# Optimization experiments

Hardware: AMD Instinct MI355X
Metric: run time of the kernel (lower is better)

Reference implementation:

```python
import jax, jax.numpy as jnp
import numpy as np

K = 8  # in-edges per non-source node (forward direction)

def _mp_forward(y, src_local, pre_w, pre_b, upd_w, upd_b):
    # y: [L, P, D] node features by topological level; src_local: [L-1, P*K]
    L, P, D = y.shape
    # level 0 has no in-edges: builtin mean gives z = 0 -> y += relu(update(0)) = relu(b)
    y0 = jax.nn.relu(upd_b) + y[0]
    def step(y_prev, inp):
        src, y_init = inp
        msg = jax.nn.relu(y_prev[src] @ pre_w + pre_b)      # [P*K, D] gather + msg FNN
        z = msg.reshape(P, K, D).mean(axis=1)               # fn.mean reduce
        y_new = jax.nn.relu(z @ upd_w + upd_b) + y_init     # update + residual
        return y_new, y_new
    _, ys = jax.lax.scan(step, y0, (src_local, y[1:]))
    return jnp.concatenate([y0[None], ys], axis=0)

def _mp_reverse(y, src_local, pre_w, pre_b, upd_w, upd_b):
    # propagate along reversed edges, reverse topological order
    L, P, D = y.shape
    dst_local = jnp.repeat(jnp.arange(P), K)                # local dst of each fwd edge
    y_last = jax.nn.relu(upd_b) + y[-1]                     # sinks: z = 0
    def step(y_next, inp):
        src, y_init = inp
        msg = jax.nn.relu(y_next[dst_local] @ pre_w + pre_b)            # [P*K, D]
        z_sum = jax.ops.segment_sum(msg, src, num_segments=P)
        deg = jax.ops.segment_sum(jnp.ones((P * K,), msg.dtype), src, num_segments=P)
        z = z_sum / jnp.maximum(deg, 1.0)[:, None]          # mean; zero-deg -> 0
        y_new = jax.nn.relu(z @ upd_w + upd_b) + y_init
        return y_new, y_new
    _, ys = jax.lax.scan(step, y_last, (src_local, y[:-1]), reverse=True)
    return jnp.concatenate([ys, y_last[None]], axis=0)

def setup_inputs() -> dict:
    key = jax.random.key(0)
    ks = jax.random.split(key, 16)
    N, node_dim, D = 131072, 128, 128   # D = out_dim // 2
    L, P = 16, 8192
    s = 0.06
    return {
        "x": jax.random.normal(ks[0], (N, node_dim), jnp.float32),
        "src_local": jax.random.randint(ks[1], (L - 1, P * K), 0, P).astype(jnp.int32),
        "nt_w1": jax.random.normal(ks[2], (node_dim, node_dim), jnp.float32) * s,
        "nt_b1": jax.random.normal(ks[3], (node_dim,), jnp.float32) * s,
        "nt_w2": jax.random.normal(ks[4], (node_dim, D), jnp.float32) * s,
        "nt_b2": jax.random.normal(ks[5], (D,), jnp.float32) * s,
        "f_pre_w": jax.random.normal(ks[6], (D, D), jnp.float32) * s,
        "f_pre_b": jax.random.normal(ks[7], (D,), jnp.float32) * s,
        "f_upd_w": jax.random.normal(ks[8], (D, D), jnp.float32) * s,
        "f_upd_b": jax.random.normal(ks[9], (D,), jnp.float32) * s,
        "b_pre_w": jax.random.normal(ks[10], (D, D), jnp.float32) * s,
        "b_pre_b": jax.random.normal(ks[11], (D,), jnp.float32) * s,
        "b_upd_w": jax.random.normal(ks[12], (D, D), jnp.float32) * s,
        "b_upd_b": jax.random.normal(ks[13], (D,), jnp.float32) * s,
    }

def reference(x, src_local, nt_w1, nt_b1, nt_w2, nt_b2,
              f_pre_w, f_pre_b, f_upd_w, f_upd_b,
              b_pre_w, b_pre_b, b_upd_w, b_upd_b):
    Lm1, PK = src_local.shape
    P, L = PK // K, Lm1 + 1
    N = x.shape[0]
    # node_transform: FNN(node_dim, [node_dim], out_dim//2)
    h = jax.nn.relu(x @ nt_w1 + nt_b1) @ nt_w2 + nt_b2      # [N, D]
    y = h.reshape(L, P, -1)
    hf = _mp_forward(y, src_local, f_pre_w, f_pre_b, f_upd_w, f_upd_b).reshape(N, -1)
    hb = _mp_reverse(y, src_local, b_pre_w, b_pre_b, b_upd_w, b_upd_b).reshape(N, -1)
    return jnp.concatenate([hf, hb], axis=1)
```

## Files before the change

### kernel.cpp

```cpp
#include <hip/hip_runtime.h>
#include <cstddef>
#include <cstdint>

#define DD   128
#define PP   8192
#define KK   8
#define LLV  16
#define NN   131072
#define NE   65536
#define NLVL 15

typedef _Float16 h8 __attribute__((ext_vector_type(8)));
typedef _Float16 h4 __attribute__((ext_vector_type(4)));
typedef float f4v __attribute__((ext_vector_type(4)));

__device__ __forceinline__ float4 ld4(const float* p) { return *(const float4*)p; }
__device__ __forceinline__ void st4(float* p, float4 v) { *(float4*)p = v; }

__device__ __forceinline__ int swz(int row, int k) { return row * 128 + (k ^ ((row & 7) << 3)); }

__device__ __forceinline__ void hstore4(_Float16* ah, int row, int k0, float4 v) {
  int o = swz(row, k0);
  h4 hi;
  hi[0] = (_Float16)v.x; hi[1] = (_Float16)v.y;
  hi[2] = (_Float16)v.z; hi[3] = (_Float16)v.w;
  *(h4*)(ah + o) = hi;
}

__device__ __forceinline__ void load_bfrags1(const _Float16* __restrict__ img, int t16, int lane,
                                             h8 Bh[4], h8 Bl[4]) {
#pragma unroll
  for (int ks = 0; ks < 4; ks++) {
    int o = ((t16 * 4 + ks) * 64 + lane) * 8;
    Bh[ks] = *(const h8*)(img + o);
    Bl[ks] = *(const h8*)(img + 16384 + o);
  }
}

__device__ __forceinline__ f4v gemm_rt(const _Float16* __restrict__ ah,
                                       const h8 Bh[4], const h8 Bl[4], int rbase, int lane) {
  int r16 = lane & 15, kb = lane >> 4;
  int arow = rbase + r16;
  h8 Ah[4];
#pragma unroll
  for (int ks = 0; ks < 4; ks++) Ah[ks] = *(const h8*)(ah + swz(arow, ks * 32 + kb * 8));
  f4v a = {0.f, 0.f, 0.f, 0.f};
#pragma unroll
  for (int ks = 0; ks < 4; ks++) a = __builtin_amdgcn_mfma_f32_16x16x32_f16(Ah[ks], Bh[ks], a, 0, 0, 0);
#pragma unroll
  for (int ks = 0; ks < 4; ks++) a = __builtin_amdgcn_mfma_f32_16x16x32_f16(Ah[ks], Bl[ks], a, 0, 0, 0);
  return a;
}

__global__ __launch_bounds__(1024) void setup_kernel(
    const float* __restrict__ w0, const float* __restrict__ w1,
    const float* __restrict__ w2, const float* __restrict__ w3,
    const float* __restrict__ w4, const float* __restrict__ w5,
    _Float16* __restrict__ img_base,
    const int* __restrict__ src_all,
    int* __restrict__ offs, int* __restrict__ edges) {
  int t = threadIdx.x;
  if (blockIdx.x < 12) {
    int mat = blockIdx.x >> 1;
    int g = (blockIdx.x & 1) * 1024 + t;
    const float* w;
    switch (mat) {
      case 0: w = w0; break;
      case 1: w = w1; break;
      case 2: w = w2; break;
      case 3: w = w3; break;
      case 4: w = w4; break;
      default: w = w5; break;
    }
    _Float16* img = img_base + (size_t)mat * 32768;
    int t16 = g >> 8, ks = (g >> 6) & 3, lane = g & 63;
    int n = t16 * 16 + (lane & 15);
    int kb = ks * 32 + (lane >> 4) * 8;
    h8 hi, lo;
#pragma unroll
    for (int j = 0; j < 8; j++) {
      float v = w[(kb + j) * 128 + n];
      _Float16 h = (_Float16)v;
      hi[j] = h;
      lo[j] = (_Float16)(v - (float)h);
    }
    int o = ((t16 * 4 + ks) * 64 + lane) * 8;
    *(h8*)(img + o) = hi;
    *(h8*)(img + 16384 + o) = lo;
  } else {
    int l = blockIdx.x - 12;
    const int* src = src_all + (size_t)l * NE;
    __shared__ int cnt[PP];
    __shared__ int bsum[1024];
#pragma unroll
    for (int j = 0; j < 8; j++) cnt[t + j * 1024] = 0;
    __syncthreads();
#pragma unroll 4
    for (int j = 0; j < 64; j++) {
      int q = src[j * 1024 + t];
      atomicAdd(&cnt[q], 1);
    }
    __syncthreads();
    int loc[8];
    int s = 0;
#pragma unroll
    for (int j = 0; j < 8; j++) { loc[j] = cnt[t * 8 + j]; s += loc[j]; }
    bsum[t] = s;
    __syncthreads();
    for (int off = 1; off < 1024; off <<= 1) {
      int v = (t >= off) ? bsum[t - off] : 0;
      __syncthreads();
      bsum[t] += v;
      __syncthreads();
    }
    int run = (t == 0) ? 0 : bsum[t - 1];
#pragma unroll
    for (int j = 0; j < 8; j++) {
      offs[l * (PP + 1) + t * 8 + j] = run;
      cnt[t * 8 + j] = run;
      run += loc[j];
    }
    if (t == 1023) offs[l * (PP + 1) + PP] = run;
    __syncthreads();
#pragma unroll 4
    for (int j = 0; j < 64; j++) {
      int e = j * 1024 + t;
      int q = src[e];
      int pos = atomicAdd(&cnt[q], 1);
      edges[(size_t)l * NE + pos] = e >> 3;
    }
  }
}

__global__ __launch_bounds__(512, 4) void nt_kernel(
    const float* __restrict__ x,
    const _Float16* __restrict__ w1img, const float* __restrict__ b1,
    const _Float16* __restrict__ w2img, const float* __restrict__ b2,
    float* __restrict__ hout,
    const float* __restrict__ f_upd_b, const _Float16* __restrict__ f_pre_img,
    const float* __restrict__ f_pre_b,
    const float* __restrict__ b_upd_b, const _Float16* __restrict__ b_pre_img,
    const float* __restrict__ b_pre_b,
    _Float16* __restrict__ mf0, _Float16* __restrict__ mb0,
    float* __restrict__ out) {
  __shared__ __align__(16) _Float16 abuf0[8192];
  __shared__ __align__(16) _Float16 abuf1[8192];
  int tid = threadIdx.x;
  int lane = tid & 63, wv = tid >> 6;
  int r16 = lane & 15, kb = lane >> 4;
  int colg = wv * 16 + r16;
  size_t base = (size_t)blockIdx.x * 64;

  h8 Bh[4], Bl[4];
  load_bfrags1(w1img, wv, lane, Bh, Bl);

#pragma unroll
  for (int j = 0; j < 4; j++) {
    int s = tid + j * 512;
    float4 v = ((const float4*)(x + base * 128))[s];
    hstore4(abuf0, s >> 5, (s & 31) * 4, v);
  }
  __syncthreads();

  f4v acc[4];
#pragma unroll
  for (int rt = 0; rt < 4; rt++) acc[rt] = gemm_rt(abuf0, Bh, Bl, rt * 16, lane);
  load_bfrags1(w2img, wv, lane, Bh, Bl);
  {
    float b = b1[colg];
#pragma unroll
    for (int rt = 0; rt < 4; rt++)
#pragma unroll
      for (int r = 0; r < 4; r++)
        abuf1[swz(rt * 16 + kb * 4 + r, colg)] = (_Float16)fmaxf(acc[rt][r] + b, 0.f);
  }
  __syncthreads();

#pragma unroll
  for (int rt = 0; rt < 4; rt++) acc[rt] = gemm_rt(abuf1, Bh, Bl, rt * 16, lane);
  float b2s = b2[colg];
#pragma unroll
  for (int rt = 0; rt < 4; rt++)
#pragma unroll
    for (int r = 0; r < 4; r++) {
      int row = rt * 16 + kb * 4 + r;
      hout[(base + row) * 128 + colg] = acc[rt][r] + b2s;
    }

  bool lvl0 = (blockIdx.x < 128);
  bool lvl15 = (blockIdx.x >= 1920);
  if (lvl0 || lvl15) {
    const float* ub = lvl0 ? f_upd_b : b_upd_b;
    const _Float16* pimg = lvl0 ? f_pre_img : b_pre_img;
    const float* pb = lvl0 ? f_pre_b : b_pre_b;
    _Float16* mdst = lvl0 ? mf0 : mb0;
    int coloff = lvl0 ? 0 : 128;
    size_t lbase = lvl0 ? 0 : (size_t)15 * PP;

    float rb = fmaxf(ub[colg], 0.f);
#pragma unroll
    for (int rt = 0; rt < 4; rt++)
#pragma unroll
      for (int r = 0; r < 4; r++) {
        int row = rt * 16 + kb * 4 + r;
        float u0 = (acc[rt][r] + b2s) + rb;
        out[(base + row) * 256 + coloff + colg] = u0;
        abuf0[swz(row, colg)] = (_Float16)u0;
      }
    load_bfrags1(pimg, wv, lane, Bh, Bl);
    __syncthreads();
#pragma unroll
    for (int rt = 0; rt < 4; rt++) acc[rt] = gemm_rt(abuf0, Bh, Bl, rt * 16, lane);
    float pbs = pb[colg];
#pragma unroll
    for (int rt = 0; rt < 4; rt++)
#pragma unroll
      for (int r = 0; r < 4; r++) {
        int row = rt * 16 + kb * 4 + r;
        float m = fmaxf(acc[rt][r] + pbs, 0.f);
        mdst[(base + row - lbase) * 128 + colg] = (_Float16)m;
      }
  }
}

__global__ __launch_bounds__(512, 4) void mp_step(
    const float* __restrict__ h,
    const int* __restrict__ src_all,
    const int* __restrict__ offs,
    const int* __restrict__ edges,
    const _Float16* __restrict__ fw_upd_img, const float* __restrict__ fw_upd_b,
    const _Float16* __restrict__ fw_pre_img, const float* __restrict__ fw_pre_b,
    const _Float16* __restrict__ bw_upd_img, const float* __restrict__ bw_upd_b,
    const _Float16* __restrict__ bw_pre_img, const float* __restrict__ bw_pre_b,
    const _Float16* __restrict__ mf_in, _Float16* __restrict__ mf_out,
    const _Float16* __restrict__ mb_in, _Float16* __restrict__ mb_out,
    float* __restrict__ out, int step) {
  __shared__ __align__(16) _Float16 abuf0[4096];
  __shared__ __align__(16) _Float16 abuf1[4096];
  int tid = threadIdx.x;
  int lane = tid & 63, wv = tid >> 6;
  int c4 = tid & 31, rg2 = (tid >> 5) * 2;
  int r16 = lane & 15, kb = lane >> 4;
  int colg = wv * 16 + r16;
  bool is_fwd = blockIdx.x < 256;
  int tile = (blockIdx.x & 255) * 32;
  int level = is_fwd ? step : 15 - step;
  const _Float16* upd_img = is_fwd ? fw_upd_img : bw_upd_img;
  const float* upd_b = is_fwd ? fw_upd_b : bw_upd_b;
  const _Float16* pre_img = is_fwd ? fw_pre_img : bw_pre_img;
  const float* pre_b = is_fwd ? fw_pre_b : bw_pre_b;
  const _Float16* m_in = is_fwd ? mf_in : mb_in;
  _Float16* m_out      = is_fwd ? mf_out : mb_out;
  bool has_mout = (step < 15);
  int col_off = is_fwd ? 0 : 128;

  float hreg[2][4];
#pragma unroll
  for (int rt = 0; rt < 2; rt++)
#pragma unroll
    for (int r = 0; r < 4; r++) {
      int row = rt * 16 + kb * 4 + r;
      hreg[rt][r] = h[((size_t)level * PP + tile + row) * 128 + colg];
    }

  h8 BhU[4], BlU[4];
  load_bfrags1(upd_img, wv, lane, BhU, BlU);

  if (is_fwd) {
    const int* src = src_all + (size_t)(step - 1) * NE;
#pragma unroll
    for (int i = 0; i < 2; i++) {
      int r = rg2 + i;
      int p = tile + r;
      const int4* sp = (const int4*)(src + p * 8);
      int4 s0 = sp[0], s1 = sp[1];
      h4 v0 = *(const h4*)(m_in + (size_t)s0.x * 128 + c4 * 4);
      h4 v1 = *(const h4*)(m_in + (size_t)s0.y * 128 + c4 * 4);
      h4 v2 = *(const h4*)(m_in + (size_t)s0.z * 128 + c4 * 4);
      h4 v3 = *(const h4*)(m_in + (size_t)s0.w * 128 + c4 * 4);
      h4 v4 = *(const h4*)(m_in + (size_t)s1.x * 128 + c4 * 4);
      h4 v5 = *(const h4*)(m_in + (size_t)s1.y * 128 + c4 * 4);
      h4 v6 = *(const h4*)(m_in + (size_t)s1.z * 128 + c4 * 4);
      h4 v7 = *(const h4*)(m_in + (size_t)s1.w * 128 + c4 * 4);
      float4 a;
      a.x = (((float)v0[0] + (float)v1[0]) + ((float)v2[0] + (float)v3[0])) +
            (((float)v4[0] + (float)v5[0]) + ((float)v6[0] + (float)v7[0]));
      a.y = (((float)v0[1] + (float)v1[1]) + ((float)v2[1] + (float)v3[1])) +
            (((float)v4[1] + (float)v5[1]) + ((float)v6[1] + (float)v7[1]));
      a.z = (((float)v0[2] + (float)v1[2]) + ((float)v2[2] + (float)v3[2])) +
            (((float)v4[2] + (float)v5[2]) + ((float)v6[2] + (float)v7[2]));
      a.w = (((float)v0[3] + (float)v1[3]) + ((float)v2[3] + (float)v3[3])) +
            (((float)v4[3] + (float)v5[3]) + ((float)v6[3] + (float)v7[3]));
      a.x *= 0.125f; a.y *= 0.125f; a.z *= 0.125f; a.w *= 0.125f;
      hstore4(abuf0, r, c4 * 4, a);
    }
  } else {
    const int* off_l = offs + level * (PP + 1);
    const int* ep = edges + level * NE;
#pragma unroll
    for (int i = 0; i < 2; i++) {
      int r = rg2 + i;
      int q = tile + r;
      int e0 = off_l[q], e1 = off_l[q + 1];
      float4 a = {0.f, 0.f, 0.f, 0.f};
      int idx = e0;
      for (; idx + 4 <= e1; idx += 4) {
        int p0 = ep[idx], p1 = ep[idx + 1], p2 = ep[idx + 2], p3 = ep[idx + 3];
        h4 v0 = *(const h4*)(m_in + (size_t)p0 * 128 + c4 * 4);
        h4 v1 = *(const h4*)(m_in + (size_t)p1 * 128 + c4 * 4);
        h4 v2 = *(const h4*)(m_in + (size_t)p2 * 128 + c4 * 4);
        h4 v3 = *(const h4*)(m_in + (size_t)p3 * 128 + c4 * 4);
        a.x += ((float)v0[0] + (float)v1[0]) + ((float)v2[0] + (float)v3[0]);
        a.y += ((float)v0[1] + (float)v1[1]) + ((float)v2[1] + (float)v3[1]);
        a.z += ((float)v0[2] + (float)v1[2]) + ((float)v2[2] + (float)v3[2]);
        a.w += ((float)v0[3] + (float)v1[3]) + ((float)v2[3] + (float)v3[3]);
      }
      for (; idx < e1; idx++) {
        int p = ep[idx];
        h4 v = *(const h4*)(m_in + (size_t)p * 128 + c4 * 4);
        a.x += (float)v[0]; a.y += (float)v[1]; a.z += (float)v[2]; a.w += (float)v[3];
      }
      float inv = (e1 > e0) ? 1.0f / (float)(e1 - e0) : 0.f;
      a.x *= inv; a.y *= inv; a.z *= inv; a.w *= inv;
      hstore4(abuf0, r, c4 * 4, a);
    }
  }
  __syncthreads();

  f4v acc[2];
#pragma unroll
  for (int rt = 0; rt < 2; rt++) acc[rt] = gemm_rt(abuf0, BhU, BlU, rt * 16, lane);
  {
    float ubs = upd_b[colg];
#pragma unroll
    for (int rt = 0; rt < 2; rt++)
#pragma unroll
      for (int r = 0; r < 4; r++) {
        int row = rt * 16 + kb * 4 + r;
        size_t n = (size_t)level * PP + tile + row;
        float uval = fmaxf(acc[rt][r] + ubs, 0.f) + hreg[rt][r];
        out[n * 256 + col_off + colg] = uval;
        abuf1[swz(row, colg)] = (_Float16)uval;
      }
  }

  if (has_mout) {
    h8 BhP[4], BlP[4];
    load_bfrags1(pre_img, wv, lane, BhP, BlP);
    __syncthreads();
#pragma unroll
    for (int rt = 0; rt < 2; rt++) acc[rt] = gemm_rt(abuf1, BhP, BlP, rt * 16, lane);
    float pbs = pre_b[colg];
#pragma unroll
    for (int rt = 0; rt < 2; rt++)
#pragma unroll
      for (int r = 0; r < 4; r++) {
        int row = rt * 16 + kb * 4 + r;
        float m = fmaxf(acc[rt][r] + pbs, 0.f);
        m_out[(size_t)(tile + row) * 128 + colg] = (_Float16)m;
      }
  }
}

extern "C" void kernel_launch(void* const* d_in, const int* in_sizes, int n_in,
                              void* d_out, int out_size, void* d_ws, size_t ws_size,
                              hipStream_t stream) {
  const float* x      = (const float*)d_in[0];
  const int*   src    = (const int*)d_in[1];
  const float* nt_w1  = (const float*)d_in[2];
  const float* nt_b1  = (const float*)d_in[3];
  const float* nt_w2  = (const float*)d_in[4];
  const float* nt_b2  = (const float*)d_in[5];
  const float* f_pre_w = (const float*)d_in[6];
  const float* f_pre_b = (const float*)d_in[7];
  const float* f_upd_w = (const float*)d_in[8];
  const float* f_upd_b = (const float*)d_in[9];
  const float* b_pre_w = (const float*)d_in[10];
  const float* b_pre_b = (const float*)d_in[11];
  const float* b_upd_w = (const float*)d_in[12];
  const float* b_upd_b = (const float*)d_in[13];
  float* out = (float*)d_out;

  float* wsf = (float*)d_ws;
  float* h   = wsf;
  _Float16* mf0 = (_Float16*)(h + (size_t)NN * DD);
  _Float16* mf1 = mf0 + (size_t)PP * DD;
  _Float16* mb0 = mf1 + (size_t)PP * DD;
  _Float16* mb1 = mb0 + (size_t)PP * DD;
  int* offs   = (int*)(mb1 + (size_t)PP * DD);
  int* edges  = offs + NLVL * (PP + 1);

  uintptr_t ip = (uintptr_t)(edges + (size_t)NLVL * NE);
  ip = (ip + 15) & ~(uintptr_t)15;
  _Float16* img = (_Float16*)ip;
  _Float16* i_ntw1 = img;
  _Float16* i_ntw2 = img + 32768;
  _Float16* i_fupd = img + 2 * 32768;
  _Float16* i_fpre = img + 3 * 32768;
  _Float16* i_bupd = img + 4 * 32768;
  _Float16* i_bpre = img + 5 * 32768;

  setup_kernel<<<27, 1024, 0, stream>>>(nt_w1, nt_w2, f_upd_w, f_pre_w, b_upd_w, b_pre_w,
                                        img, src, offs, edges);
  nt_kernel<<<NN / 64, 512, 0, stream>>>(x, i_ntw1, nt_b1, i_ntw2, nt_b2, h,
                                         f_upd_b, i_fpre, f_pre_b,
                                         b_upd_b, i_bpre, b_pre_b,
                                         mf0, mb0, out);

  for (int s = 1; s < 16; s++) {
    const _Float16* mf_in = (s & 1) ? mf0 : mf1;
    _Float16* mf_out      = (s & 1) ? mf1 : mf0;
    const _Float16* mb_in = (s & 1) ? mb0 : mb1;
    _Float16* mb_out      = (s & 1) ? mb1 : mb0;
    mp_step<<<512, 512, 0, stream>>>(h, src, offs, edges,
                                     i_fupd, f_upd_b, i_fpre, f_pre_b,
                                     i_bupd, b_upd_b, i_bpre, b_pre_b,
                                     mf_in, mf_out, mb_in, mb_out, out, s);
  }
}
```

Before: 525.3 us.

## Load-balance reverse-direction edge aggregation across warps via LDS float atomics

The reverse pass now splits the whole tile's CSR edge range evenly across 16 thread groups instead of giving each group fixed rows with variable degree. Each group scatters gathered messages into a shared-memory float buffer with atomicAdd, using the destination row packed into the high bits of each edge entry. The aim is to remove the load imbalance that random in-degrees cause. The cost is LDS atomic contention, an extra 16KB of shared memory that may lower occupancy, and a non-deterministic summation order. Separately, the MFMA chain in the GEMM helper is split into two independent accumulators to shorten the dependency chain.

New measurement: 1.145 ms. +117.9%, slower.

```diff
diff --git a/kernel.cpp b/kernel.cpp
--- a/kernel.cpp
+++ b/kernel.cpp
@@ -44,12 +44,19 @@
   h8 Ah[4];
 #pragma unroll
   for (int ks = 0; ks < 4; ks++) Ah[ks] = *(const h8*)(ah + swz(arow, ks * 32 + kb * 8));
-  f4v a = {0.f, 0.f, 0.f, 0.f};
-#pragma unroll
-  for (int ks = 0; ks < 4; ks++) a = __builtin_amdgcn_mfma_f32_16x16x32_f16(Ah[ks], Bh[ks], a, 0, 0, 0);
-#pragma unroll
-  for (int ks = 0; ks < 4; ks++) a = __builtin_amdgcn_mfma_f32_16x16x32_f16(Ah[ks], Bl[ks], a, 0, 0, 0);
-  return a;
+  f4v a0 = {0.f, 0.f, 0.f, 0.f};
+  f4v a1 = {0.f, 0.f, 0.f, 0.f};
+#pragma unroll
+  for (int ks = 0; ks < 2; ks++) {
+    a0 = __builtin_amdgcn_mfma_f32_16x16x32_f16(Ah[ks], Bh[ks], a0, 0, 0, 0);
+    a1 = __builtin_amdgcn_mfma_f32_16x16x32_f16(Ah[ks + 2], Bh[ks + 2], a1, 0, 0, 0);
+  }
+#pragma unroll
+  for (int ks = 0; ks < 2; ks++) {
+    a0 = __builtin_amdgcn_mfma_f32_16x16x32_f16(Ah[ks], Bl[ks], a0, 0, 0, 0);
+    a1 = __builtin_amdgcn_mfma_f32_16x16x32_f16(Ah[ks + 2], Bl[ks + 2], a1, 0, 0, 0);
+  }
+  return a0 + a1;
 }
 
 __global__ __launch_bounds__(1024) void setup_kernel(
@@ -127,7 +134,7 @@
       int e = j * 1024 + t;
       int q = src[e];
       int pos = atomicAdd(&cnt[q], 1);
-      edges[(size_t)l * NE + pos] = e >> 3;
+      edges[(size_t)l * NE + pos] = (e >> 3) | ((q & 31) << 16);
     }
   }
 }
@@ -237,6 +244,7 @@
     float* __restrict__ out, int step) {
   __shared__ __align__(16) _Float16 abuf0[4096];
   __shared__ __align__(16) _Float16 abuf1[4096];
+  __shared__ __align__(16) float zbuf[4096];
   int tid = threadIdx.x;
   int lane = tid & 63, wv = tid >> 6;
   int c4 = tid & 31, rg2 = (tid >> 5) * 2;
@@ -294,38 +302,61 @@
       a.x *= 0.125f; a.y *= 0.125f; a.z *= 0.125f; a.w *= 0.125f;
       hstore4(abuf0, r, c4 * 4, a);
     }
+    __syncthreads();
   } else {
+#pragma unroll
+    for (int i = 0; i < 2; i++)
+      *(float4*)(zbuf + (rg2 + i) * 128 + c4 * 4) = float4{0.f, 0.f, 0.f, 0.f};
+    __syncthreads();
+
     const int* off_l = offs + level * (PP + 1);
     const int* ep = edges + level * NE;
+    int e0b = off_l[tile], e1b = off_l[tile + 32];
+    int cnt = e1b - e0b;
+    int slot = tid >> 5;
+    int per = (cnt + 15) >> 4;
+    int ea = e0b + slot * per;
+    int eb = ea + per; if (eb > e1b) eb = e1b;
+    int e = ea;
+    for (; e + 4 <= eb; e += 4) {
+      int v0i = ep[e], v1i = ep[e + 1], v2i = ep[e + 2], v3i = ep[e + 3];
+      h4 m0 = *(const h4*)(m_in + (size_t)(v0i & 0xFFFF) * 128 + c4 * 4);
+      h4 m1 = *(const h4*)(m_in + (size_t)(v1i & 0xFFFF) * 128 + c4 * 4);
+      h4 m2 = *(const h4*)(m_in + (size_t)(v2i & 0xFFFF) * 128 + c4 * 4);
+      h4 m3 = *(const h4*)(m_in + (size_t)(v3i & 0xFFFF) * 128 + c4 * 4);
+      int b0 = (v0i >> 16) * 128 + c4 * 4;
+      int b1 = (v1i >> 16) * 128 + c4 * 4;
+      int b2 = (v2i >> 16) * 128 + c4 * 4;
+      int b3 = (v3i >> 16) * 128 + c4 * 4;
+#pragma unroll
+      for (int j = 0; j < 4; j++) {
+        atomicAdd(&zbuf[b0 + j], (float)m0[j]);
+        atomicAdd(&zbuf[b1 + j], (float)m1[j]);
+        atomicAdd(&zbuf[b2 + j], (float)m2[j]);
+        atomicAdd(&zbuf[b3 + j], (float)m3[j]);
+      }
+    }
+    for (; e < eb; e++) {
+      int vi = ep[e];
+      h4 m = *(const h4*)(m_in + (size_t)(vi & 0xFFFF) * 128 + c4 * 4);
+      int b = (vi >> 16) * 128 + c4 * 4;
+#pragma unroll
+      for (int j = 0; j < 4; j++) atomicAdd(&zbuf[b + j], (float)m[j]);
+    }
+    __syncthreads();
+
 #pragma unroll
     for (int i = 0; i < 2; i++) {
       int r = rg2 + i;
       int q = tile + r;
-      int e0 = off_l[q], e1 = off_l[q + 1];
-      float4 a = {0.f, 0.f, 0.f, 0.f};
-      int idx = e0;
-      for (; idx + 4 <= e1; idx += 4) {
-        int p0 = ep[idx], p1 = ep[idx + 1], p2 = ep[idx + 2], p3 = ep[idx + 3];
-        h4 v0 = *(const h4*)(m_in + (size_t)p0 * 128 + c4 * 4);
-        h4 v1 = *(const h4*)(m_in + (size_t)p1 * 128 + c4 * 4);
-        h4 v2 = *(const h4*)(m_in + (size_t)p2 * 128 + c4 * 4);
-        h4 v3 = *(const h4*)(m_in + (size_t)p3 * 128 + c4 * 4);
-        a.x += ((float)v0[0] + (float)v1[0]) + ((float)v2[0] + (float)v3[0]);
-        a.y += ((float)v0[1] + (float)v1[1]) + ((float)v2[1] + (float)v3[1]);
-        a.z += ((float)v0[2] + (float)v1[2]) + ((float)v2[2] + (float)v3[2]);
-        a.w += ((float)v0[3] + (float)v1[3]) + ((float)v2[3] + (float)v3[3]);
-      }
-      for (; idx < e1; idx++) {
-        int p = ep[idx];
-        h4 v = *(const h4*)(m_in + (size_t)p * 128 + c4 * 4);
-        a.x += (float)v[0]; a.y += (float)v[1]; a.z += (float)v[2]; a.w += (float)v[3];
-      }
-      float inv = (e1 > e0) ? 1.0f / (float)(e1 - e0) : 0.f;
+      int deg = off_l[q + 1] - off_l[q];
+      float inv = (deg > 0) ? 1.0f / (float)deg : 0.f;
+      float4 a = *(const float4*)(zbuf + r * 128 + c4 * 4);
       a.x *= inv; a.y *= inv; a.z *= inv; a.w *= inv;
       hstore4(abuf0, r, c4 * 4, a);
     }
-  }
-  __syncthreads();
+    __syncthreads();
+  }
 
   f4v acc[2];
 #pragma unroll
```
